# Kernel optimization log

Measured on AMD Instinct MI355X. Metric: run time of the kernel, lower is better.

Reference implementation:

```python
import jax, jax.numpy as jnp
import numpy as np

EPS = 1e-5
HEADS, DK, DV = 8, 32, 32


def conv3x3(x, w, b):
    # regular (non-depthwise, despite the name) 3x3 conv, stride 1, padding 1
    y = jax.lax.conv_general_dilated(
        x, w, window_strides=(1, 1), padding='SAME',
        dimension_numbers=('NCHW', 'OIHW', 'NCHW'))
    return y + b[None, :, None, None]


def setup_inputs() -> dict:
    key = jax.random.key(0)
    ks = jax.random.split(key, 16)
    C = 256
    d = {}
    d['x'] = jax.random.normal(ks[0], (8, C, 32, 32), jnp.float32)
    s_lin = 1.0 / np.sqrt(C)
    s_conv = 1.0 / np.sqrt(C * 9)
    d['Wq'] = jax.random.normal(ks[1], (C, HEADS * DK), jnp.float32) * s_lin
    d['bq'] = jnp.zeros((HEADS * DK,), jnp.float32)
    d['conv_k_w'] = jax.random.normal(ks[2], (C, C, 3, 3), jnp.float32) * s_conv
    d['conv_k_b'] = jnp.zeros((C,), jnp.float32)
    d['Wk'] = jax.random.normal(ks[3], (C, HEADS * DK), jnp.float32) * s_lin
    d['bk'] = jnp.zeros((HEADS * DK,), jnp.float32)
    d['conv_v_w'] = jax.random.normal(ks[4], (C, C, 3, 3), jnp.float32) * s_conv
    d['conv_v_b'] = jnp.zeros((C,), jnp.float32)
    d['Wv'] = jax.random.normal(ks[5], (C, HEADS * DV), jnp.float32) * s_lin
    d['bv'] = jnp.zeros((HEADS * DV,), jnp.float32)
    d['Wo'] = jax.random.normal(ks[6], (HEADS * DV, C), jnp.float32) * s_lin
    d['bo'] = jnp.zeros((C,), jnp.float32)
    d['B'] = jax.random.normal(ks[7], (1, HEADS, 1024, 1024), jnp.float32) * 0.02
    return d


def reference(x, Wq, bq, conv_k_w, conv_k_b, Wk, bk, conv_v_w, conv_v_b, Wv, bv, Wo, bo, B):
    b, c, h, w = x.shape
    hw = h * w
    xr = x.reshape(b, c, hw).transpose(0, 2, 1)  # [b, hw, c]
    # F.layer_norm with normalized_shape == full shape: whole-tensor stats, no affine
    m = jnp.mean(xr)
    v = jnp.mean((xr - m) ** 2)
    xn = (xr - m) * jax.lax.rsqrt(v + EPS)

    q = (xn @ Wq + bq).reshape(b, hw, HEADS, DK).transpose(0, 2, 1, 3)  # [b,H,hw,dk]

    k = conv3x3(x, conv_k_w, conv_k_b)  # stride 1 -> same spatial size (per source)
    k = k.reshape(b, c, hw).transpose(0, 2, 1)
    k = (k @ Wk + bk).reshape(b, hw, HEADS, DK).transpose(0, 2, 1, 3)

    vv = conv3x3(x, conv_v_w, conv_v_b)
    vv = vv.reshape(b, c, hw).transpose(0, 2, 1)
    vv = (vv @ Wv + bv).reshape(b, hw, HEADS, DV).transpose(0, 2, 1, 3)

    scale = DK ** (-0.5)
    attn = jnp.einsum('bhid,bhjd->bhij', q, k) * scale + B  # [b,H,hw,hw]
    attn = jax.nn.softmax(attn, axis=-1)
    out = jnp.einsum('bhij,bhjd->bhid', attn, vv)  # [b,H,hw,dv]
    out = out.transpose(0, 2, 1, 3).reshape(b, hw, HEADS * DV)
    out = out @ Wo + bo  # [b, hw, c]
    # faithful to torch .view(b, c, h, w): raw reshape, NO transpose
    out = out.reshape(b, c, h, w)
    return out + x
```

## Files before the change

### kernel.cpp

```cpp
#include <hip/hip_runtime.h>
#include <hip/hip_bf16.h>
#include <math.h>

#define B_     8
#define C_     256
#define HW_    1024
#define NTOT   (B_*C_*HW_)
#define HEADS_ 8
#define DK_    32
#define SCALE_ 0.17677669529663687f

#define F_STATS 0
#define F_PART  16
#define F_YK2   8192
#define F_YV2   (F_YK2 + NTOT)
#define F_XB    (F_YV2 + NTOT)
#define F_WT    (F_XB + NTOT/2)
#define F_QB    (F_WT + 589824)
#define F_KB    (F_QB + NTOT/2)
#define F_VT    (F_KB + NTOT/2)

typedef float f32x4 __attribute__((ext_vector_type(4)));
typedef short short8 __attribute__((ext_vector_type(8)));

__device__ __forceinline__ short bf16s(float f) {
    __hip_bfloat16 h = __float2bfloat16(f);
    return *(short*)&h;
}
__device__ __forceinline__ unsigned pack_bf16(float a, float b) {
    unsigned ua = (unsigned short)bf16s(a);
    unsigned ub = (unsigned short)bf16s(b);
    return ua | (ub << 16);
}
__device__ __forceinline__ void gload_lds16(const short* g, short* l) {
    __builtin_amdgcn_global_load_lds(
        (const __attribute__((address_space(1))) unsigned*)g,
        (__attribute__((address_space(3))) unsigned*)l, 16, 0, 0);
}

__global__ void k_prep_x(const float* __restrict__ x, short* __restrict__ xb,
                         float* __restrict__ part) {
    __shared__ short t[64 * 258];
    __shared__ float ls[4], ls2[4];
    int b = blockIdx.x >> 4, p0 = (blockIdx.x & 15) << 6;
    int tid = threadIdx.x;
    float s = 0.f, s2 = 0.f;
    for (int i = tid; i < 256 * 64; i += 256) {
        int ci = i >> 6, p = i & 63;
        float v = x[(b * C_ + ci) * HW_ + p0 + p];
        s += v; s2 += v * v;
        t[p * 258 + ci] = bf16s(v);
    }
    for (int o = 32; o; o >>= 1) { s += __shfl_down(s, o); s2 += __shfl_down(s2, o); }
    int wid = tid >> 6, lane = tid & 63;
    if (lane == 0) { ls[wid] = s; ls2[wid] = s2; }
    __syncthreads();
    if (tid == 0) {
        float a = 0.f, bb = 0.f;
        for (int i = 0; i < 4; i++) { a += ls[i]; bb += ls2[i]; }
        part[blockIdx.x * 2] = a; part[blockIdx.x * 2 + 1] = bb;
    }
    for (int i = tid; i < 64 * 256; i += 256) {
        int p = i >> 8, ci = i & 255;
        xb[(b * HW_ + p0 + p) * C_ + ci] = t[p * 258 + ci];
    }
}

__global__ void k_stats(const float* __restrict__ part, float* __restrict__ stats) {
    __shared__ float ls[256], ls2[256];
    float s = 0.f, s2 = 0.f;
    for (int i = threadIdx.x; i < 128; i += 256) { s += part[2 * i]; s2 += part[2 * i + 1]; }
    ls[threadIdx.x] = s; ls2[threadIdx.x] = s2;
    __syncthreads();
    for (int off = 128; off; off >>= 1) {
        if (threadIdx.x < off) { ls[threadIdx.x] += ls[threadIdx.x + off]; ls2[threadIdx.x] += ls2[threadIdx.x + off]; }
        __syncthreads();
    }
    if (threadIdx.x == 0) {
        float m = ls[0] / (float)NTOT;
        float var = ls2[0] / (float)NTOT - m * m;
        stats[0] = m;
        stats[1] = rsqrtf(var + 1e-5f);
    }
}

__global__ void k_prep_w(const float* __restrict__ wk, const float* __restrict__ wv,
                         short* __restrict__ wt) {
    int idx = blockIdx.x * 256 + threadIdx.x;
    int ci0 = (idx << 2) & 255;
    int rest = idx >> 6;
    int n = rest & 511, tap = rest >> 9;
    const float* src = (n < 256) ? (wk + (n * C_) * 9) : (wv + ((n - 256) * C_) * 9);
    short4 o;
    short* op = (short*)&o;
    for (int u = 0; u < 4; u++)
        op[u] = bf16s(src[(ci0 + u) * 9 + tap]);
    *(short4*)&wt[((tap * 512 + n) * C_) + ci0] = o;
}

__global__ void k_prep_pw(const float* __restrict__ Wq, const float* __restrict__ Wk,
                          const float* __restrict__ Wv, const float* __restrict__ Wo,
                          short* __restrict__ wt4) {
    __shared__ short t[64 * 66];
    int mi = blockIdx.x >> 4, tl = blockIdx.x & 15;
    int c0 = (tl >> 2) * 64, e0 = (tl & 3) * 64;
    const float* W = mi == 0 ? Wq : mi == 1 ? Wk : mi == 2 ? Wv : Wo;
    int tid = threadIdx.x;
    for (int i = tid; i < 4096; i += 256) {
        int cl = i >> 6, el = i & 63;
        t[cl * 66 + el] = bf16s(W[(c0 + cl) * 256 + e0 + el]);
    }
    __syncthreads();
    for (int i = tid; i < 4096; i += 256) {
        int el = i >> 6, cl = i & 63;
        wt4[mi * 65536 + (e0 + el) * 256 + c0 + cl] = t[cl * 66 + el];
    }
}

__global__ void k_prep_beta(const float* __restrict__ Wq, const float* __restrict__ bq,
                            const float* __restrict__ stats, float* __restrict__ beta0) {
    __shared__ float ps[1024];
    int t = threadIdx.x, e = t & 255, part = t >> 8;
    float s = 0.f;
    for (int c = part * 64; c < part * 64 + 64; c++) s += Wq[c * 256 + e];
    ps[t] = s;
    __syncthreads();
    if (t < 256) {
        float cs = ps[t] + ps[t + 256] + ps[t + 512] + ps[t + 768];
        beta0[t] = (bq[t] - stats[0] * stats[1] * cs) * SCALE_;
    }
}

__device__ __forceinline__ int a_off(int slot, int chunk) {
    int c = chunk ^ (slot & 3);
    int s = slot ^ ((slot >> 2) & 1);
    return s * 64 + c * 16;
}

__global__ __launch_bounds__(512, 4)
void k_conv_mfma(const short* __restrict__ xb, const short* __restrict__ wt,
                 const float* __restrict__ bk, const float* __restrict__ bv,
                 float* __restrict__ yk2, float* __restrict__ yv2) {
    __shared__ short a_sh[204 * 32];
    __shared__ short b_sh[9 * 2048];
    int bid = blockIdx.x;
    int nt = bid & 7, pt = (bid >> 3) & 7, b = bid >> 6;
    int R0 = pt * 4;
    int tid = threadIdx.x;
    int w = tid >> 6, l = tid & 63;
    int wm = w >> 1, wn = w & 1;
    int col16 = l & 15, kq = l >> 4;

    int offs[2], loffs[2];
    #pragma unroll
    for (int it = 0; it < 2; it++) {
        int i = tid + it * 512;
        if (i < 816) {
            int slot = i >> 2, chunk = i & 3;
            int ty = slot / 34, tx = slot - ty * 34;
            int Y = R0 - 1 + ty, X = tx - 1;
            offs[it] = ((unsigned)Y < 32u && (unsigned)X < 32u)
                       ? ((b * HW_ + Y * 32 + X) * C_ + chunk * 8) : -1;
            loffs[it] = a_off(slot, chunk);
        } else { offs[it] = -1; loffs[it] = -1; }
    }

    int bgoff[5];
    int nbj = 0;
    #pragma unroll 1
    for (int j = w; j < 36; j += 8) {
        int S = j * 64 + l;
        int tap = S >> 8, s = S & 255;
        int colb = s >> 2, kqs = s & 3;
        int kq2 = kqs ^ ((colb >> 1) & 3);
        bgoff[nbj++] = (tap * 512 + nt * 64 + colb) * C_ + kq2 * 8;
    }

    f32x4 acc[2][2];
    #pragma unroll
    for (int m = 0; m < 2; m++)
        #pragma unroll
        for (int n = 0; n < 2; n++) acc[m][n] = (f32x4)0.f;

    int sr[2];
    #pragma unroll
    for (int nf = 0; nf < 2; nf++) {
        int colb = wn * 32 + nf * 16 + col16;
        sr[nf] = (colb << 2) | (kq ^ ((colb >> 1) & 3));
    }

    {
        short8 sv[2];
        #pragma unroll
        for (int it = 0; it < 2; it++)
            sv[it] = (offs[it] >= 0) ? *(const short8*)(xb + offs[it]) : (short8)0;
        int jj = 0;
        #pragma unroll 1
        for (int j = w; j < 36; j += 8, jj++)
            gload_lds16(wt + bgoff[jj], b_sh + j * 512);
        #pragma unroll
        for (int it = 0; it < 2; it++)
            if (loffs[it] >= 0) *(short8*)((char*)a_sh + loffs[it]) = sv[it];
    }
    __syncthreads();

    #pragma unroll 1
    for (int step = 0; step < 8; step++) {
        const char* ab = (const char*)a_sh;
        const char* bbp = (const char*)b_sh;
        #pragma unroll
        for (int tap = 0; tap < 9; tap++) {
            const int dyi = tap / 3, dxi = tap % 3;
            short8 af[2], bf[2];
            #pragma unroll
            for (int mf = 0; mf < 2; mf++) {
                int slot = (wm + dyi) * 34 + mf * 16 + col16 + dxi;
                af[mf] = *(const short8*)(ab + a_off(slot, kq));
            }
            #pragma unroll
            for (int nf = 0; nf < 2; nf++)
                bf[nf] = *(const short8*)(bbp + tap * 4096 + sr[nf] * 16);
            #pragma unroll
            for (int mf = 0; mf < 2; mf++)
                #pragma unroll
                for (int nf = 0; nf < 2; nf++)
                    acc[mf][nf] = __builtin_amdgcn_mfma_f32_16x16x32_bf16(af[mf], bf[nf], acc[mf][nf], 0, 0, 0);
        }
        if (step < 7) {
            int ci0n = step * 32 + 32;
            __syncthreads();
            short8 sv[2];
            #pragma unroll
            for (int it = 0; it < 2; it++)
                sv[it] = (offs[it] >= 0) ? *(const short8*)(xb + offs[it] + ci0n) : (short8)0;
            int jj = 0;
            #pragma unroll 1
            for (int j = w; j < 36; j += 8, jj++)
                gload_lds16(wt + bgoff[jj] + ci0n, b_sh + j * 512);
            #pragma unroll
            for (int it = 0; it < 2; it++)
                if (loffs[it] >= 0) *(short8*)((char*)a_sh + loffs[it]) = sv[it];
            __syncthreads();
        }
    }

    const bool isv = (nt >= 4);
    float* dst = isv ? yv2 : yk2;
    const float* bias = isv ? bv : bk;
    int cbase = (nt & 3) * 64 + wn * 32 + col16;
    #pragma unroll
    for (int nf = 0; nf < 2; nf++) {
        int co = cbase + nf * 16;
        float bi = bias[co];
        #pragma unroll
        for (int mf = 0; mf < 2; mf++) {
            #pragma unroll
            for (int r = 0; r < 4; r++) {
                int pixel = pt * 128 + wm * 32 + mf * 16 + kq * 4 + r;
                dst[(b * HW_ + pixel) * C_ + co] = acc[mf][nf][r] + bi;
            }
        }
    }
}

__global__ void k_proj_mfma(const short* __restrict__ xb,
                            const float* __restrict__ yk2, const float* __restrict__ yv2,
                            const short* __restrict__ wt4,
                            const float* __restrict__ bkp, const float* __restrict__ bvp,
                            const float* __restrict__ stats, const float* __restrict__ beta0,
                            short* __restrict__ qb, short* __restrict__ kb,
                            short* __restrict__ vt) {
    __shared__ char smem[17408];
    int pj = blockIdx.x, pt = blockIdx.y, b = blockIdx.z;
    int p0 = pt * 32;
    int tid = threadIdx.x, w = tid >> 6, l = tid & 63;
    int c16 = l & 15, kq = l >> 4;

    if (pj == 0) {
        #pragma unroll
        for (int it = 0; it < 4; it++) {
            int i = it * 256 + tid;
            int slab = i >> 7, rem = i & 127, slot = rem >> 2, chunk = rem & 3;
            short8 v = *(const short8*)(xb + ((b * HW_ + p0 + slot) * C_ + slab * 32 + chunk * 8));
            *(short8*)(smem + slab * 2048 + a_off(slot, chunk)) = v;
        }
    } else {
        const float* src = (pj == 1) ? yk2 : yv2;
        #pragma unroll
        for (int it = 0; it < 4; it++) {
            int i = it * 256 + tid;
            int slab = i >> 7, rem = i & 127, slot = rem >> 2, chunk = rem & 3;
            const float* sp = src + (b * HW_ + p0 + slot) * C_ + slab * 32 + chunk * 8;
            float4 f0 = *(const float4*)sp;
            float4 f1 = *(const float4*)(sp + 4);
            short8 v;
            v[0] = bf16s(f0.x); v[1] = bf16s(f0.y); v[2] = bf16s(f0.z); v[3] = bf16s(f0.w);
            v[4] = bf16s(f1.x); v[5] = bf16s(f1.y); v[6] = bf16s(f1.z); v[7] = bf16s(f1.w);
            *(short8*)(smem + slab * 2048 + a_off(slot, chunk)) = v;
        }
    }
    __syncthreads();

    const short* wt_p = wt4 + pj * 65536;
    f32x4 acc[2][4];
    #pragma unroll
    for (int m = 0; m < 2; m++)
        #pragma unroll
        for (int n = 0; n < 4; n++) acc[m][n] = (f32x4)0.f;

    for (int s = 0; s < 8; s++) {
        short8 af[2], bf[4];
        #pragma unroll
        for (int mf = 0; mf < 2; mf++)
            af[mf] = *(const short8*)(smem + s * 2048 + a_off(mf * 16 + c16, kq));
        #pragma unroll
        for (int nf = 0; nf < 4; nf++)
            bf[nf] = *(const short8*)(wt_p + (w * 64 + nf * 16 + c16) * 256 + s * 32 + kq * 8);
        #pragma unroll
        for (int mf = 0; mf < 2; mf++)
            #pragma unroll
            for (int nf = 0; nf < 4; nf++)
                acc[mf][nf] = __builtin_amdgcn_mfma_f32_16x16x32_bf16(af[mf], bf[nf], acc[mf][nf], 0, 0, 0);
    }

    float alpha = (pj == 0) ? stats[1] * SCALE_ : 1.f;
    float beta[4];
    #pragma unroll
    for (int nf = 0; nf < 4; nf++) {
        int e = w * 64 + nf * 16 + c16;
        beta[nf] = (pj == 0) ? beta0[e] : (pj == 1 ? bkp[e] : bvp[e]);
    }
    __syncthreads();

    short* rp = (short*)smem + w * 2176;
    if (pj < 2) {
        #pragma unroll
        for (int mf = 0; mf < 2; mf++)
            #pragma unroll
            for (int nf = 0; nf < 4; nf++)
                #pragma unroll
                for (int rg = 0; rg < 4; rg++) {
                    int px = mf * 16 + kq * 4 + rg, el = nf * 16 + c16;
                    rp[px * 66 + el] = bf16s(alpha * acc[mf][nf][rg] + beta[nf]);
                }
        __syncthreads();
        short* dst = (pj == 0) ? qb : kb;
        #pragma unroll
        for (int j = 0; j < 4; j++) {
            int px = j * 8 + (l >> 3), el = (l & 7) * 8;
            short8 v = *(const short8*)(rp + px * 66 + el);
            int e = w * 64 + el, h = e >> 5, d = e & 31;
            *(short8*)(dst + ((b * 8 + h) * HW_ + p0 + px) * DK_ + d) = v;
        }
    } else {
        #pragma unroll
        for (int mf = 0; mf < 2; mf++)
            #pragma unroll
            for (int nf = 0; nf < 4; nf++)
                #pragma unroll
                for (int rg = 0; rg < 4; rg++) {
                    int px = mf * 16 + kq * 4 + rg, el = nf * 16 + c16;
                    rp[el * 34 + px] = bf16s(acc[mf][nf][rg] + beta[nf]);
                }
        __syncthreads();
        #pragma unroll
        for (int j = 0; j < 4; j++) {
            int el = j * 16 + (l >> 2), px = (l & 3) * 8;
            short8 v = *(const short8*)(rp + el * 34 + px);
            int e = w * 64 + el, h = e >> 5, d = e & 31;
            *(short8*)(vt + ((b * 8 + h) * DK_ + d) * HW_ + p0 + px) = v;
        }
    }
}

__global__ __launch_bounds__(256, 4)
void k_attn(const short* __restrict__ qb, const short* __restrict__ kb,
            const short* __restrict__ vt, const float* __restrict__ Bb,
            short* __restrict__ ao) {
    __shared__ __align__(16) short Ks[128 * 32];
    __shared__ __align__(16) short Vs[32 * 128];
    __shared__ __align__(16) short Ps[4][16 * 128];
    int bid = blockIdx.x;
    int h = bid & 7, b = (bid >> 3) & 7, qt = bid >> 6;
    int bh = b * HEADS_ + h;
    int tid = threadIdx.x, w = tid >> 6, l = tid & 63;
    int g = l >> 4, c16 = l & 15;

    int qrow = qt * 64 + w * 16 + c16;
    short8 qf = *(const short8*)(qb + (bh * HW_ + qrow) * DK_ + g * 8);

    const float* Brow = Bb + (h * HW_ + qrow) * HW_;
    float m_run = -1e30f, l_run = 0.f;
    f32x4 ot[2];
    ot[0] = (f32x4)0.f; ot[1] = (f32x4)0.f;
    char* pbase = (char*)&Ps[w][0];

    int vrow = tid >> 4, vch = tid & 15;
    int vrow2 = (tid + 256) >> 4, vch2 = (tid + 256) & 15;

    short8 kreg[2], vreg[2];
    kreg[0] = *(const short8*)(kb + (bh * HW_) * DK_ + tid * 8);
    kreg[1] = *(const short8*)(kb + (bh * HW_) * DK_ + (tid + 256) * 8);
    vreg[0] = *(const short8*)(vt + (bh * DK_ + vrow) * HW_ + vch * 8);
    vreg[1] = *(const short8*)(vt + (bh * DK_ + vrow2) * HW_ + vch2 * 8);

    for (int kv0 = 0; kv0 < HW_; kv0 += 128) {
        __syncthreads();
        *(short8*)(Ks + tid * 8) = kreg[0];
        *(short8*)(Ks + (tid + 256) * 8) = kreg[1];
        *(short8*)((char*)Vs + vrow * 256 + ((vch * 16) ^ ((vrow & 7) << 4))) = vreg[0];
        *(short8*)((char*)Vs + vrow2 * 256 + ((vch2 * 16) ^ ((vrow2 & 7) << 4))) = vreg[1];
        __syncthreads();
        if (kv0 + 128 < HW_) {
            int nk = kv0 + 128;
            kreg[0] = *(const short8*)(kb + (bh * HW_ + nk) * DK_ + tid * 8);
            kreg[1] = *(const short8*)(kb + (bh * HW_ + nk) * DK_ + (tid + 256) * 8);
            vreg[0] = *(const short8*)(vt + (bh * DK_ + vrow) * HW_ + nk + vch * 8);
            vreg[1] = *(const short8*)(vt + (bh * DK_ + vrow2) * HW_ + nk + vch2 * 8);
        }

        f32x4 st[8];
        __builtin_amdgcn_s_setprio(1);
        #pragma unroll
        for (int mt = 0; mt < 8; mt++) {
            float4 bi = *(const float4*)(Brow + kv0 + mt * 16 + g * 4);
            f32x4 acc; acc[0] = bi.x; acc[1] = bi.y; acc[2] = bi.z; acc[3] = bi.w;
            short8 kf = *(const short8*)(Ks + (mt * 16 + c16) * DK_ + g * 8);
            st[mt] = __builtin_amdgcn_mfma_f32_16x16x32_bf16(kf, qf, acc, 0, 0, 0);
        }
        __builtin_amdgcn_s_setprio(0);

        float pmax = st[0][0];
        #pragma unroll
        for (int mt = 0; mt < 8; mt++)
            #pragma unroll
            for (int rg = 0; rg < 4; rg++) pmax = fmaxf(pmax, st[mt][rg]);
        pmax = fmaxf(pmax, __shfl_xor(pmax, 16));
        pmax = fmaxf(pmax, __shfl_xor(pmax, 32));
        if (!__all(pmax <= m_run + 8.f)) {
            float mnew = fmaxf(m_run, pmax);
            float f = __expf(m_run - mnew);
            m_run = mnew;
            l_run *= f;
            int fv = __float_as_int(f);
            #pragma unroll
            for (int rg = 0; rg < 4; rg++) {
                float fr = __int_as_float(__builtin_amdgcn_ds_bpermute((g * 4 + rg) << 2, fv));
                ot[0][rg] *= fr;
                ot[1][rg] *= fr;
            }
        }
        float s = 0.f;
        #pragma unroll
        for (int mt = 0; mt < 8; mt++)
            #pragma unroll
            for (int rg = 0; rg < 4; rg++) {
                float e_ = __expf(st[mt][rg] - m_run);
                st[mt][rg] = e_;
                s += e_;
            }
        s += __shfl_xor(s, 16);
        s += __shfl_xor(s, 32);
        l_run += s;

        #pragma unroll
        for (int mt = 0; mt < 8; mt++) {
            unsigned lo = pack_bf16(st[mt][0], st[mt][1]);
            unsigned hi = pack_bf16(st[mt][2], st[mt][3]);
            unsigned long long pr = (unsigned long long)lo | ((unsigned long long)hi << 32);
            *(unsigned long long*)(pbase + c16 * 256 + ((mt * 32 + g * 8) ^ ((c16 & 7) << 4))) = pr;
        }
        __builtin_amdgcn_s_setprio(1);
        #pragma unroll
        for (int kt = 0; kt < 4; kt++) {
            short8 pf = *(const short8*)(pbase + c16 * 256 + ((kt * 64 + g * 16) ^ ((c16 & 7) << 4)));
            #pragma unroll
            for (int nt = 0; nt < 2; nt++) {
                short8 vf = *(const short8*)((char*)Vs + (c16 + 16 * nt) * 256 + ((kt * 64 + g * 16) ^ ((c16 & 7) << 4)));
                ot[nt] = __builtin_amdgcn_mfma_f32_16x16x32_bf16(pf, vf, ot[nt], 0, 0, 0);
            }
        }
        __builtin_amdgcn_s_setprio(0);
    }

    float linv = 1.f / l_run;
    int lrv = __float_as_int(linv);
    #pragma unroll
    for (int rg = 0; rg < 4; rg++) {
        float li = __int_as_float(__builtin_amdgcn_ds_bpermute((g * 4 + rg) << 2, lrv));
        int qg = qt * 64 + w * 16 + g * 4 + rg;
        #pragma unroll
        for (int nt = 0; nt < 2; nt++)
            ao[(b * HW_ + qg) * C_ + h * DK_ + nt * 16 + c16] = bf16s(ot[nt][rg] * li);
    }
}

__global__ void k_out_mfma(const short* __restrict__ aob, const short* __restrict__ wot,
                           const float* __restrict__ bo, const float* __restrict__ x,
                           float* __restrict__ out) {
    __shared__ char smem[16384];
    int pt = blockIdx.x, b = blockIdx.y;
    int p0 = pt * 32;
    int tid = threadIdx.x, w = tid >> 6, l = tid & 63;
    int c16 = l & 15, kq = l >> 4;

    #pragma unroll
    for (int it = 0; it < 4; it++) {
        int i = it * 256 + tid;
        int slab = i >> 7, rem = i & 127, slot = rem >> 2, chunk = rem & 3;
        short8 v = *(const short8*)(aob + ((b * HW_ + p0 + slot) * C_ + slab * 32 + chunk * 8));
        *(short8*)(smem + slab * 2048 + a_off(slot, chunk)) = v;
    }
    __syncthreads();

    f32x4 acc[2][4];
    #pragma unroll
    for (int m = 0; m < 2; m++)
        #pragma unroll
        for (int n = 0; n < 4; n++) acc[m][n] = (f32x4)0.f;

    for (int s = 0; s < 8; s++) {
        short8 af[2], bf[4];
        #pragma unroll
        for (int mf = 0; mf < 2; mf++)
            af[mf] = *(const short8*)(smem + s * 2048 + a_off(mf * 16 + c16, kq));
        #pragma unroll
        for (int nf = 0; nf < 4; nf++)
            bf[nf] = *(const short8*)(wot + (w * 64 + nf * 16 + c16) * 256 + s * 32 + kq * 8);
        #pragma unroll
        for (int mf = 0; mf < 2; mf++)
            #pragma unroll
            for (int nf = 0; nf < 4; nf++)
                acc[mf][nf] = __builtin_amdgcn_mfma_f32_16x16x32_bf16(af[mf], bf[nf], acc[mf][nf], 0, 0, 0);
    }

    #pragma unroll
    for (int nf = 0; nf < 4; nf++) {
        int e = w * 64 + nf * 16 + c16;
        float bov = bo[e];
        #pragma unroll
        for (int mf = 0; mf < 2; mf++) {
            #pragma unroll
            for (int rg = 0; rg < 4; rg++) {
                int px = mf * 16 + kq * 4 + rg;
                int idx = b * (C_ * HW_) + (p0 + px) * 256 + e;
                out[idx] = acc[mf][nf][rg] + bov + x[idx];
            }
        }
    }
}

extern "C" void kernel_launch(void* const* d_in, const int* in_sizes, int n_in,
                              void* d_out, int out_size, void* d_ws, size_t ws_size,
                              hipStream_t stream) {
    const float* x   = (const float*)d_in[0];
    const float* Wq  = (const float*)d_in[1];
    const float* bq  = (const float*)d_in[2];
    const float* ckw = (const float*)d_in[3];
    const float* ckb = (const float*)d_in[4];
    const float* Wk  = (const float*)d_in[5];
    const float* bk  = (const float*)d_in[6];
    const float* cvw = (const float*)d_in[7];
    const float* cvb = (const float*)d_in[8];
    const float* Wv  = (const float*)d_in[9];
    const float* bv  = (const float*)d_in[10];
    const float* Wo  = (const float*)d_in[11];
    const float* bo  = (const float*)d_in[12];
    const float* Bb  = (const float*)d_in[13];
    float* ws  = (float*)d_ws;
    float* out = (float*)d_out;

    short* xb      = (short*)(ws + F_XB);
    short* wt      = (short*)(ws + F_WT);
    short* wt4     = (short*)(ws + F_WT);
    float* beta0   = ws + F_WT + 131072;
    short* qb      = (short*)(ws + F_QB);
    short* kb      = (short*)(ws + F_KB);
    short* vt      = (short*)(ws + F_VT);
    short* aob     = (short*)(ws + F_YK2);
    short* wot     = wt4 + 3 * 65536;

    k_prep_x   <<<128,  256, 0, stream>>>(x, xb, ws + F_PART);
    k_stats    <<<1,    256, 0, stream>>>(ws + F_PART, ws + F_STATS);
    k_prep_w   <<<1152, 256, 0, stream>>>(ckw, cvw, wt);
    k_conv_mfma<<<512,  512, 0, stream>>>(xb, wt, ckb, cvb, ws + F_YK2, ws + F_YV2);
    k_prep_pw  <<<64,   256, 0, stream>>>(Wq, Wk, Wv, Wo, wt4);
    k_prep_beta<<<1,   1024, 0, stream>>>(Wq, bq, ws + F_STATS, beta0);
    k_proj_mfma<<<dim3(3, 32, 8), 256, 0, stream>>>(xb, ws + F_YK2, ws + F_YV2,
                                                    wt4, bk, bv, ws + F_STATS, beta0,
                                                    qb, kb, vt);
    k_attn     <<<1024, 256, 0, stream>>>(qb, kb, vt, Bb, aob);
    k_out_mfma <<<dim3(32, 8), 256, 0, stream>>>(aob, wot, bo, x, out);
}
```

Before: 145.9 us.

## Keep P in registers, load K via direct-to-LDS, prefetch bias into registers

```diff
diff --git a/kernel.cpp b/kernel.cpp
--- a/kernel.cpp
+++ b/kernel.cpp
@@ -379,7 +379,6 @@
             short* __restrict__ ao) {
     __shared__ __align__(16) short Ks[128 * 32];
     __shared__ __align__(16) short Vs[32 * 128];
-    __shared__ __align__(16) short Ps[4][16 * 128];
     int bid = blockIdx.x;
     int h = bid & 7, b = (bid >> 3) & 7, qt = bid >> 6;
     int bh = b * HEADS_ + h;
@@ -388,47 +387,48 @@
 
     int qrow = qt * 64 + w * 16 + c16;
     short8 qf = *(const short8*)(qb + (bh * HW_ + qrow) * DK_ + g * 8);
-
     const float* Brow = Bb + (h * HW_ + qrow) * HW_;
+
+    float4 breg[8];
+    #pragma unroll
+    for (int mt = 0; mt < 8; mt++)
+        breg[mt] = *(const float4*)(Brow + mt * 16 + g * 4);
+
     float m_run = -1e30f, l_run = 0.f;
     f32x4 ot[2];
     ot[0] = (f32x4)0.f; ot[1] = (f32x4)0.f;
-    char* pbase = (char*)&Ps[w][0];
 
     int vrow = tid >> 4, vch = tid & 15;
     int vrow2 = (tid + 256) >> 4, vch2 = (tid + 256) & 15;
-
-    short8 kreg[2], vreg[2];
-    kreg[0] = *(const short8*)(kb + (bh * HW_) * DK_ + tid * 8);
-    kreg[1] = *(const short8*)(kb + (bh * HW_) * DK_ + (tid + 256) * 8);
-    vreg[0] = *(const short8*)(vt + (bh * DK_ + vrow) * HW_ + vch * 8);
-    vreg[1] = *(const short8*)(vt + (bh * DK_ + vrow2) * HW_ + vch2 * 8);
+    const short* kbase = kb + bh * HW_ * DK_;
 
     for (int kv0 = 0; kv0 < HW_; kv0 += 128) {
         __syncthreads();
-        *(short8*)(Ks + tid * 8) = kreg[0];
-        *(short8*)(Ks + (tid + 256) * 8) = kreg[1];
-        *(short8*)((char*)Vs + vrow * 256 + ((vch * 16) ^ ((vrow & 7) << 4))) = vreg[0];
-        *(short8*)((char*)Vs + vrow2 * 256 + ((vch2 * 16) ^ ((vrow2 & 7) << 4))) = vreg[1];
+        gload_lds16(kbase + kv0 * DK_ + (w * 2) * 512 + l * 8, Ks + (w * 2) * 512);
+        gload_lds16(kbase + kv0 * DK_ + (w * 2 + 1) * 512 + l * 8, Ks + (w * 2 + 1) * 512);
+        {
+            short8 v0 = *(const short8*)(vt + (bh * DK_ + vrow) * HW_ + kv0 + vch * 8);
+            short8 v1 = *(const short8*)(vt + (bh * DK_ + vrow2) * HW_ + kv0 + vch2 * 8);
+            *(short8*)((char*)Vs + vrow * 256 + ((vch * 16) ^ ((vrow & 7) << 4))) = v0;
+            *(short8*)((char*)Vs + vrow2 * 256 + ((vch2 * 16) ^ ((vrow2 & 7) << 4))) = v1;
+        }
         __syncthreads();
-        if (kv0 + 128 < HW_) {
-            int nk = kv0 + 128;
-            kreg[0] = *(const short8*)(kb + (bh * HW_ + nk) * DK_ + tid * 8);
-            kreg[1] = *(const short8*)(kb + (bh * HW_ + nk) * DK_ + (tid + 256) * 8);
-            vreg[0] = *(const short8*)(vt + (bh * DK_ + vrow) * HW_ + nk + vch * 8);
-            vreg[1] = *(const short8*)(vt + (bh * DK_ + vrow2) * HW_ + nk + vch2 * 8);
-        }
 
         f32x4 st[8];
         __builtin_amdgcn_s_setprio(1);
         #pragma unroll
         for (int mt = 0; mt < 8; mt++) {
-            float4 bi = *(const float4*)(Brow + kv0 + mt * 16 + g * 4);
-            f32x4 acc; acc[0] = bi.x; acc[1] = bi.y; acc[2] = bi.z; acc[3] = bi.w;
+            f32x4 acc;
+            acc[0] = breg[mt].x; acc[1] = breg[mt].y; acc[2] = breg[mt].z; acc[3] = breg[mt].w;
             short8 kf = *(const short8*)(Ks + (mt * 16 + c16) * DK_ + g * 8);
             st[mt] = __builtin_amdgcn_mfma_f32_16x16x32_bf16(kf, qf, acc, 0, 0, 0);
         }
         __builtin_amdgcn_s_setprio(0);
+        if (kv0 + 128 < HW_) {
+            #pragma unroll
+            for (int mt = 0; mt < 8; mt++)
+                breg[mt] = *(const float4*)(Brow + kv0 + 128 + mt * 16 + g * 4);
+        }
 
         float pmax = st[0][0];
         #pragma unroll
@@ -463,21 +463,33 @@
         s += __shfl_xor(s, 32);
         l_run += s;
 
-        #pragma unroll
-        for (int mt = 0; mt < 8; mt++) {
-            unsigned lo = pack_bf16(st[mt][0], st[mt][1]);
-            unsigned hi = pack_bf16(st[mt][2], st[mt][3]);
-            unsigned long long pr = (unsigned long long)lo | ((unsigned long long)hi << 32);
-            *(unsigned long long*)(pbase + c16 * 256 + ((mt * 32 + g * 8) ^ ((c16 & 7) << 4))) = pr;
-        }
+        short8 pa[4];
+        #pragma unroll
+        for (int kt = 0; kt < 4; kt++) {
+            unsigned u0 = pack_bf16(st[2 * kt][0], st[2 * kt][1]);
+            unsigned u1 = pack_bf16(st[2 * kt][2], st[2 * kt][3]);
+            unsigned u2 = pack_bf16(st[2 * kt + 1][0], st[2 * kt + 1][1]);
+            unsigned u3 = pack_bf16(st[2 * kt + 1][2], st[2 * kt + 1][3]);
+            unsigned* pu = (unsigned*)&pa[kt];
+            pu[0] = u0; pu[1] = u1; pu[2] = u2; pu[3] = u3;
+        }
+
         __builtin_amdgcn_s_setprio(1);
         #pragma unroll
         for (int kt = 0; kt < 4; kt++) {
-            short8 pf = *(const short8*)(pbase + c16 * 256 + ((kt * 64 + g * 16) ^ ((c16 & 7) << 4)));
             #pragma unroll
             for (int nt = 0; nt < 2; nt++) {
-                short8 vf = *(const short8*)((char*)Vs + (c16 + 16 * nt) * 256 + ((kt * 64 + g * 16) ^ ((c16 & 7) << 4)));
-                ot[nt] = __builtin_amdgcn_mfma_f32_16x16x32_bf16(pf, vf, ot[nt], 0, 0, 0);
+                int dv = c16 + 16 * nt;
+                int X0 = kt * 64 + 8 * g;
+                int X1 = X0 + 32;
+                int a0 = dv * 256 + ((((X0 >> 4) ^ (dv & 7)) << 4) | (X0 & 15));
+                int a1 = dv * 256 + ((((X1 >> 4) ^ (dv & 7)) << 4) | (X1 & 15));
+                unsigned long long lo = *(const unsigned long long*)((char*)Vs + a0);
+                unsigned long long hi = *(const unsigned long long*)((char*)Vs + a1);
+                short8 vf;
+                *(unsigned long long*)&vf = lo;
+                *((unsigned long long*)&vf + 1) = hi;
+                ot[nt] = __builtin_amdgcn_mfma_f32_16x16x32_bf16(pa[kt], vf, ot[nt], 0, 0, 0);
             }
         }
         __builtin_amdgcn_s_setprio(0);
```

Result: no change. 143.1 us (-1.9%).
